# Performance work log

Measured on AMD Instinct MI355X. Metric: run time of the kernel, lower is better.

## Reference

```python
import jax, jax.numpy as jnp
import numpy as np

N_NODES = 50000
N_EDGES = 800000
IN_CH, HID_CH, OUT_CH = 128, 256, 256
N_LAYERS = 3


def setup_inputs() -> dict:
    key = jax.random.key(0)
    ks = jax.random.split(key, 9)
    x = jax.random.normal(ks[0], (N_NODES, IN_CH), dtype=jnp.float32)
    edge_index = jax.random.randint(ks[1], (2, N_EDGES), 0, N_NODES, dtype=jnp.int32)
    # Linear params, Kaiming-ish scale
    W1 = jax.random.normal(ks[2], (IN_CH, HID_CH), dtype=jnp.float32) / np.float32(np.sqrt(IN_CH))
    b1 = jnp.zeros((HID_CH,), jnp.float32)
    W2 = jax.random.normal(ks[3], (HID_CH, HID_CH), dtype=jnp.float32) / np.float32(np.sqrt(HID_CH))
    b2 = jnp.zeros((HID_CH,), jnp.float32)
    W3 = jax.random.normal(ks[4], (HID_CH, OUT_CH), dtype=jnp.float32) / np.float32(np.sqrt(HID_CH))
    b3 = jnp.zeros((OUT_CH,), jnp.float32)
    # learnable eps per GINConv (train_eps=True); small nonzero values for a nontrivial test
    eps = jax.random.normal(ks[5], (N_LAYERS,), dtype=jnp.float32) * 0.01
    return {"x": x, "edge_index": edge_index, "W1": W1, "b1": b1,
            "W2": W2, "b2": b2, "W3": W3, "b3": b3, "eps": eps}


def _gin_conv(x, src, dst, eps, W, b):
    # sum aggregation over incoming edges: agg[i] = sum_{(j->i)} x[j]
    agg = jax.ops.segment_sum(x[src], dst, num_segments=N_NODES)
    h = (1.0 + eps) * x + agg
    return h @ W + b


def reference(x, edge_index, W1, b1, W2, b2, W3, b3, eps):
    src, dst = edge_index[0], edge_index[1]
    # layers 0..L-2: conv -> relu -> dropout (identity in eval mode)
    h = jax.nn.relu(_gin_conv(x, src, dst, eps[0], W1, b1))
    h = jax.nn.relu(_gin_conv(h, src, dst, eps[1], W2, b2))
    # final layer: no relu
    out = _gin_conv(h, src, dst, eps[2], W3, b3)
    return out
```

## Files before the change

kernel.cpp:

```cpp
#include <hip/hip_runtime.h>


typedef __attribute__((ext_vector_type(8))) short short8;
typedef __attribute__((ext_vector_type(4))) float f32x4;

__device__ inline unsigned short f2bf(float f) {
    union { float f; unsigned u; } v; v.f = f;
    unsigned r = v.u + 0x7fffu + ((v.u >> 16) & 1u);
    return (unsigned short)(r >> 16);
}
__device__ inline float bflo(unsigned u) { return __uint_as_float(u << 16); }
__device__ inline float bfhi(unsigned u) { return __uint_as_float(u & 0xffff0000u); }

__device__ __forceinline__ void gload_lds16(const unsigned short* g, unsigned short* l) {
    __builtin_amdgcn_global_load_lds(
        (const __attribute__((address_space(1))) unsigned int*)g,
        (__attribute__((address_space(3))) unsigned int*)l,
        16, 0, 0);
}

#define ACC8(v) { acc[0]+=bflo(v.x); acc[1]+=bfhi(v.x); acc[2]+=bflo(v.y); acc[3]+=bfhi(v.y); \
                  acc[4]+=bflo(v.z); acc[5]+=bfhi(v.z); acc[6]+=bflo(v.w); acc[7]+=bfhi(v.w); }

__global__ __launch_bounds__(256) void prep_kernel(
    const float* __restrict__ x, const int* __restrict__ dst,
    const float* __restrict__ W1, const float* __restrict__ W2,
    const float* __restrict__ W3,
    unsigned short* __restrict__ xb, int* __restrict__ cnt,
    unsigned short* __restrict__ Ws1, unsigned short* __restrict__ Ws2,
    unsigned short* __restrict__ Ws3, int M, int nE)
{
    const int i  = blockIdx.x * 256 + threadIdx.x;
    const int nx = M * 16;
    if (i < nx) {
        const float4* xf = reinterpret_cast<const float4*>(x);
        float4 a = xf[2*i], b = xf[2*i + 1];
        uint4 o;
        o.x = (unsigned)f2bf(a.x) | ((unsigned)f2bf(a.y) << 16);
        o.y = (unsigned)f2bf(a.z) | ((unsigned)f2bf(a.w) << 16);
        o.z = (unsigned)f2bf(b.x) | ((unsigned)f2bf(b.y) << 16);
        o.w = (unsigned)f2bf(b.z) | ((unsigned)f2bf(b.w) << 16);
        reinterpret_cast<uint4*>(xb)[i] = o;
    } else if (i < nx + nE) {
        atomicAdd(&cnt[dst[i - nx]], 1);
    } else {
        int j = i - nx - nE;
        const float* W; unsigned short* D;
        if (j < 32768)       { W = W1; D = Ws1; }
        else if (j < 98304)  { W = W2; D = Ws2; j -= 32768; }
        else if (j < 163840) { W = W3; D = Ws3; j -= 98304; }
        else return;
        const int k = j >> 8, n = j & 255;
        D[((size_t)(k >> 3) * 256 + n) * 8 + (k & 7)] = f2bf(W[(size_t)k * 256 + n]);
    }
}


__global__ __launch_bounds__(1024) void scan1_kernel(
    const int* __restrict__ cnt, int* __restrict__ excl,
    int* __restrict__ bsum, int n)
{
    __shared__ int sh[1024];
    const int tid = threadIdx.x;
    const int i = blockIdx.x * 1024 + tid;
    int v = (i < n) ? cnt[i] : 0;
    sh[tid] = v;
    __syncthreads();
    #pragma unroll
    for (int off = 1; off < 1024; off <<= 1) {
        int t = (tid >= off) ? sh[tid - off] : 0;
        __syncthreads();
        sh[tid] += t;
        __syncthreads();
    }
    if (i < n) excl[i] = sh[tid] - v;
    if (tid == 1023) bsum[blockIdx.x] = sh[1023];
}

__global__ __launch_bounds__(1024) void scan3_kernel(
    const int* __restrict__ excl, const int* __restrict__ bsum,
    int* __restrict__ row_start, int* __restrict__ cursor,
    int n, int nE, int nbl)
{
    __shared__ int sb[64];
    const int tid = threadIdx.x;
    if (tid < 64) sb[tid] = (tid < nbl) ? bsum[tid] : 0;
    __syncthreads();
    #pragma unroll
    for (int off = 1; off < 64; off <<= 1) {
        int v = 0;
        if (tid < 64 && tid >= off) v = sb[tid - off];
        __syncthreads();
        if (tid < 64) sb[tid] += v;
        __syncthreads();
    }
    const int boff = sb[blockIdx.x] - bsum[blockIdx.x];
    const int i = blockIdx.x * 1024 + tid;
    if (i < n) {
        int v = excl[i] + boff;
        row_start[i] = v;
        cursor[i] = v;
    }
    if (i == 0) row_start[n] = nE;
}

__global__ __launch_bounds__(256) void build_adj_kernel(
    const int* __restrict__ src, const int* __restrict__ dst,
    int* __restrict__ cursor, int* __restrict__ adj, int nE)
{
    int e = blockIdx.x * 256 + threadIdx.x;
    if (e < nE) {
        int p = atomicAdd(&cursor[dst[e]], 1);
        adj[p] = src[e];
    }
}


template <int C>
__global__ __launch_bounds__(256) void aggregate_bf16(
    const unsigned short* __restrict__ X, const int* __restrict__ row_start,
    const int* __restrict__ adj, const float* __restrict__ eps_arr, int layer,
    unsigned short* __restrict__ H, int M)
{
    constexpr int TPN = C / 8;
    constexpr int NPB = 256 / TPN;
    const int node = blockIdx.x * NPB + (threadIdx.x / TPN);
    const int c8   = threadIdx.x & (TPN - 1);
    if (node >= M) return;

    const uint4* __restrict__ X4 = reinterpret_cast<const uint4*>(X);

    float acc[8] = {0.f,0.f,0.f,0.f,0.f,0.f,0.f,0.f};
    const int s0 = row_start[node];
    const int s1 = row_start[node + 1];
    const int deg = s1 - s0;

    int j = s0;
    if (deg >= 4) {
        const int jend = s0 + (deg & ~3);
        int a0 = adj[j], a1 = adj[j+1], a2 = adj[j+2], a3 = adj[j+3];
        uint4 p0 = X4[(size_t)a0 * TPN + c8];
        uint4 p1 = X4[(size_t)a1 * TPN + c8];
        uint4 p2 = X4[(size_t)a2 * TPN + c8];
        uint4 p3 = X4[(size_t)a3 * TPN + c8];
        for (j += 4; j < jend; j += 4) {
            const int b0 = adj[j], b1 = adj[j+1], b2 = adj[j+2], b3 = adj[j+3];
            const uint4 n0 = X4[(size_t)b0 * TPN + c8];
            const uint4 n1 = X4[(size_t)b1 * TPN + c8];
            const uint4 n2 = X4[(size_t)b2 * TPN + c8];
            const uint4 n3 = X4[(size_t)b3 * TPN + c8];
            ACC8(p0); ACC8(p1); ACC8(p2); ACC8(p3);
            p0 = n0; p1 = n1; p2 = n2; p3 = n3;
        }
        ACC8(p0); ACC8(p1); ACC8(p2); ACC8(p3);
    }
    for (; j < s1; ++j) {
        uint4 v = X4[(size_t)adj[j] * TPN + c8];
        ACC8(v);
    }

    const uint4 xv = X4[(size_t)node * TPN + c8];
    const float epsv = 1.0f + eps_arr[layer];
    float o[8];
    o[0] = epsv * bflo(xv.x) + acc[0]; o[1] = epsv * bfhi(xv.x) + acc[1];
    o[2] = epsv * bflo(xv.y) + acc[2]; o[3] = epsv * bfhi(xv.y) + acc[3];
    o[4] = epsv * bflo(xv.z) + acc[4]; o[5] = epsv * bfhi(xv.z) + acc[5];
    o[6] = epsv * bflo(xv.w) + acc[6]; o[7] = epsv * bfhi(xv.w) + acc[7];

    uint4 ov;
    ov.x = (unsigned)f2bf(o[0]) | ((unsigned)f2bf(o[1]) << 16);
    ov.y = (unsigned)f2bf(o[2]) | ((unsigned)f2bf(o[3]) << 16);
    ov.z = (unsigned)f2bf(o[4]) | ((unsigned)f2bf(o[5]) << 16);
    ov.w = (unsigned)f2bf(o[6]) | ((unsigned)f2bf(o[7]) << 16);
    reinterpret_cast<uint4*>(H)[(size_t)node * TPN + c8] = ov;
}


template <int CIN, int RELU, int BF16OUT>
__global__ __launch_bounds__(256) void gemm_tiled(
    const unsigned short* __restrict__ H, const unsigned short* __restrict__ Wsub,
    const float* __restrict__ bias, void* __restrict__ out, int M)
{
    constexpr int S = CIN / 32;

    __shared__ __align__(16) unsigned short As[2][4][64][8];

    const int t    = threadIdx.x;
    const int bm   = blockIdx.x * 64;
    const int w    = t >> 6, lane = t & 63;
    const int lr   = lane & 15, ko = lane >> 4;

    const int srow = t & 63;
    const int skb  = t >> 6;
    const unsigned short* aG = H + (size_t)(bm + srow) * CIN + skb * 8;

    f32x4 acc[4][4];
    #pragma unroll
    for (int fn = 0; fn < 4; ++fn) {
        const float bb = bias[w*64 + fn*16 + lr];
        #pragma unroll
        for (int fm = 0; fm < 4; ++fm) {
            acc[fm][fn][0] = bb; acc[fm][fn][1] = bb;
            acc[fm][fn][2] = bb; acc[fm][fn][3] = bb;
        }
    }

    gload_lds16(aG, &As[0][skb][srow][0]);

    int cur = 0;
    for (int s = 0; s < S; ++s) {
        __syncthreads();
        if (s + 1 < S)
            gload_lds16(aG + (s+1)*32, &As[cur ^ 1][skb][srow][0]);

        short8 af[4], bf8[4];
        #pragma unroll
        for (int fm = 0; fm < 4; ++fm)
            af[fm] = *reinterpret_cast<const short8*>(&As[cur][ko][fm*16 + lr][0]);
        #pragma unroll
        for (int fn = 0; fn < 4; ++fn)
            bf8[fn] = *reinterpret_cast<const short8*>(
                Wsub + ((size_t)(s*4 + ko) * 256 + w*64 + fn*16 + lr) * 8);
        #pragma unroll
        for (int fm = 0; fm < 4; ++fm)
            #pragma unroll
            for (int fn = 0; fn < 4; ++fn)
                acc[fm][fn] = __builtin_amdgcn_mfma_f32_16x16x32_bf16(
                    af[fm], bf8[fn], acc[fm][fn], 0, 0, 0);

        cur ^= 1;
    }

    #pragma unroll
    for (int fm = 0; fm < 4; ++fm) {
        #pragma unroll
        for (int fn = 0; fn < 4; ++fn) {
            const int col = w*64 + fn*16 + lr;
            #pragma unroll
            for (int r = 0; r < 4; ++r) {
                const int row = bm + fm*16 + ko*4 + r;
                if (row < M) {
                    float v = acc[fm][fn][r];
                    if (RELU) v = fmaxf(v, 0.f);
                    if (BF16OUT)
                        ((unsigned short*)out)[(size_t)row * 256 + col] = f2bf(v);
                    else
                        ((float*)out)[(size_t)row * 256 + col] = v;
                }
            }
        }
    }
}


extern "C" void kernel_launch(void* const* d_in, const int* in_sizes, int n_in,
                              void* d_out, int out_size, void* d_ws, size_t ws_size,
                              hipStream_t stream)
{
    const float* x   = (const float*)d_in[0];
    const int*   ei  = (const int*)  d_in[1];
    const float* W1  = (const float*)d_in[2];
    const float* b1  = (const float*)d_in[3];
    const float* W2  = (const float*)d_in[4];
    const float* b2  = (const float*)d_in[5];
    const float* W3  = (const float*)d_in[6];
    const float* b3  = (const float*)d_in[7];
    const float* eps = (const float*)d_in[8];

    const int M  = in_sizes[0] / 128;
    const int nE = in_sizes[1] / 2;
    const int Mp = ((M + 63) / 64) * 64;
    const int* srcI = ei;
    const int* dstI = ei + nE;

    char* p = (char*)d_ws;
    unsigned short* xb  = (unsigned short*)p; p += (size_t)Mp * 128 * 2;
    unsigned short* h1  = (unsigned short*)p; p += (size_t)Mp * 256 * 2;
    unsigned short* h2  = (unsigned short*)p; p += (size_t)Mp * 256 * 2;
    unsigned short* Ws1 = (unsigned short*)p; p += (size_t)128 * 256 * 2;
    unsigned short* Ws2 = (unsigned short*)p; p += (size_t)256 * 256 * 2;
    unsigned short* Ws3 = (unsigned short*)p; p += (size_t)256 * 256 * 2;
    int* cnt       = (int*)p; p += (size_t)M * 4;
    int* excl      = (int*)p; p += (size_t)M * 4;
    int* bsum      = (int*)p; p += 64 * 4;
    int* row_start = (int*)p; p += (size_t)(M + 2) * 4;
    int* cursor    = (int*)p; p += (size_t)M * 4;
    int* adj       = (int*)p; p += (size_t)nE * 4;

    const int nbl = (M + 1023) / 1024;

    hipMemsetAsync(cnt, 0, (size_t)M * sizeof(int), stream);
    {
        const int total = M * 16 + nE + 163840;
        prep_kernel<<<(total + 255) / 256, 256, 0, stream>>>(
            x, dstI, W1, W2, W3, xb, cnt, Ws1, Ws2, Ws3, M, nE);
    }
    scan1_kernel<<<nbl, 1024, 0, stream>>>(cnt, excl, bsum, M);
    scan3_kernel<<<nbl, 1024, 0, stream>>>(excl, bsum, row_start, cursor, M, nE, nbl);
    build_adj_kernel<<<(nE + 255) / 256, 256, 0, stream>>>(srcI, dstI, cursor, adj, nE);

    const int gblk = Mp / 64;

    aggregate_bf16<128><<<(M + 15) / 16, 256, 0, stream>>>(
        xb, row_start, adj, eps, 0, h1, M);
    gemm_tiled<128, 1, 1><<<gblk, 256, 0, stream>>>(h1, Ws1, b1, h2, M);

    aggregate_bf16<256><<<(M + 7) / 8, 256, 0, stream>>>(
        h2, row_start, adj, eps, 1, h1, M);
    gemm_tiled<256, 1, 1><<<gblk, 256, 0, stream>>>(h1, Ws2, b2, h2, M);

    aggregate_bf16<256><<<(M + 7) / 8, 256, 0, stream>>>(
        h2, row_start, adj, eps, 2, h1, M);
    gemm_tiled<256, 0, 0><<<gblk, 256, 0, stream>>>(h1, Ws3, b3, d_out, M);
}
```

Baseline: 303.4 us.

## Store node features in channel-sliced layout and aggregate slices per block

Node features are now stored as eight channel slices (each slice holds all nodes contiguously), both in the prep conversion and in the GEMM epilogue. A new aggregation kernel assigns each block one slice and gives each wave a set of nodes, spreading a node's edges across lane groups and combining them with cross-lane shuffle reductions. The intent is that each block gathers from a smaller working set that fits better in L2 or the caches, and that a node's edges are processed in parallel. In exchange each gather becomes an 8-byte load instead of 16 bytes, shuffle reductions are added, and the GEMM's bf16 output is written with a scattered, strided pattern.

```diff
diff --git a/kernel.cpp b/kernel.cpp
--- a/kernel.cpp
+++ b/kernel.cpp
@@ -18,9 +18,6 @@
         (__attribute__((address_space(3))) unsigned int*)l,
         16, 0, 0);
 }
-
-#define ACC8(v) { acc[0]+=bflo(v.x); acc[1]+=bfhi(v.x); acc[2]+=bflo(v.y); acc[3]+=bfhi(v.y); \
-                  acc[4]+=bflo(v.z); acc[5]+=bfhi(v.z); acc[6]+=bflo(v.w); acc[7]+=bfhi(v.w); }
 
 __global__ __launch_bounds__(256) void prep_kernel(
     const float* __restrict__ x, const int* __restrict__ dst,
@@ -40,7 +37,11 @@
         o.y = (unsigned)f2bf(a.z) | ((unsigned)f2bf(a.w) << 16);
         o.z = (unsigned)f2bf(b.x) | ((unsigned)f2bf(b.y) << 16);
         o.w = (unsigned)f2bf(b.z) | ((unsigned)f2bf(b.w) << 16);
-        reinterpret_cast<uint4*>(xb)[i] = o;
+        const int node = i >> 4;
+        const int c0   = (i & 15) * 8;
+        const int cs   = c0 >> 4;
+        const size_t idx = (size_t)cs * M * 16 + (size_t)node * 16 + (c0 & 15);
+        *reinterpret_cast<uint4*>(xb + idx) = o;
     } else if (i < nx + nE) {
         atomicAdd(&cnt[dst[i - nx]], 1);
     } else {
@@ -116,67 +117,66 @@
 }
 
 
-template <int C>
-__global__ __launch_bounds__(256) void aggregate_bf16(
-    const unsigned short* __restrict__ X, const int* __restrict__ row_start,
-    const int* __restrict__ adj, const float* __restrict__ eps_arr, int layer,
+template <int CIN>
+__global__ __launch_bounds__(256) void agg_sliced(
+    const unsigned short* __restrict__ Xcs,
+    const int* __restrict__ row_start, const int* __restrict__ adj,
+    const float* __restrict__ eps_arr, int layer,
     unsigned short* __restrict__ H, int M)
 {
-    constexpr int TPN = C / 8;
-    constexpr int NPB = 256 / TPN;
-    const int node = blockIdx.x * NPB + (threadIdx.x / TPN);
-    const int c8   = threadIdx.x & (TPN - 1);
-    if (node >= M) return;
-
-    const uint4* __restrict__ X4 = reinterpret_cast<const uint4*>(X);
-
-    float acc[8] = {0.f,0.f,0.f,0.f,0.f,0.f,0.f,0.f};
-    const int s0 = row_start[node];
-    const int s1 = row_start[node + 1];
-    const int deg = s1 - s0;
-
-    int j = s0;
-    if (deg >= 4) {
-        const int jend = s0 + (deg & ~3);
-        int a0 = adj[j], a1 = adj[j+1], a2 = adj[j+2], a3 = adj[j+3];
-        uint4 p0 = X4[(size_t)a0 * TPN + c8];
-        uint4 p1 = X4[(size_t)a1 * TPN + c8];
-        uint4 p2 = X4[(size_t)a2 * TPN + c8];
-        uint4 p3 = X4[(size_t)a3 * TPN + c8];
-        for (j += 4; j < jend; j += 4) {
-            const int b0 = adj[j], b1 = adj[j+1], b2 = adj[j+2], b3 = adj[j+3];
-            const uint4 n0 = X4[(size_t)b0 * TPN + c8];
-            const uint4 n1 = X4[(size_t)b1 * TPN + c8];
-            const uint4 n2 = X4[(size_t)b2 * TPN + c8];
-            const uint4 n3 = X4[(size_t)b3 * TPN + c8];
-            ACC8(p0); ACC8(p1); ACC8(p2); ACC8(p3);
-            p0 = n0; p1 = n1; p2 = n2; p3 = n3;
-        }
-        ACC8(p0); ACC8(p1); ACC8(p2); ACC8(p3);
-    }
-    for (; j < s1; ++j) {
-        uint4 v = X4[(size_t)adj[j] * TPN + c8];
-        ACC8(v);
-    }
-
-    const uint4 xv = X4[(size_t)node * TPN + c8];
+    constexpr int SC = CIN / 8;
+    constexpr int CL = SC / 4;
+    constexpr int EG = 64 / CL;
+    constexpr int NW = 8;
+
+    const int cs   = blockIdx.x & 7;
+    const int grp  = blockIdx.x >> 3;
+    const int wave = threadIdx.x >> 6;
+    const int lane = threadIdx.x & 63;
+    const int cl   = lane & (CL - 1);
+    const int eg   = lane / CL;
+
+    const uint2* __restrict__ X2 = reinterpret_cast<const uint2*>(Xcs);
+    const size_t sbase = (size_t)cs * M * CL;
     const float epsv = 1.0f + eps_arr[layer];
-    float o[8];
-    o[0] = epsv * bflo(xv.x) + acc[0]; o[1] = epsv * bfhi(xv.x) + acc[1];
-    o[2] = epsv * bflo(xv.y) + acc[2]; o[3] = epsv * bfhi(xv.y) + acc[3];
-    o[4] = epsv * bflo(xv.z) + acc[4]; o[5] = epsv * bfhi(xv.z) + acc[5];
-    o[6] = epsv * bflo(xv.w) + acc[6]; o[7] = epsv * bfhi(xv.w) + acc[7];
-
-    uint4 ov;
-    ov.x = (unsigned)f2bf(o[0]) | ((unsigned)f2bf(o[1]) << 16);
-    ov.y = (unsigned)f2bf(o[2]) | ((unsigned)f2bf(o[3]) << 16);
-    ov.z = (unsigned)f2bf(o[4]) | ((unsigned)f2bf(o[5]) << 16);
-    ov.w = (unsigned)f2bf(o[6]) | ((unsigned)f2bf(o[7]) << 16);
-    reinterpret_cast<uint4*>(H)[(size_t)node * TPN + c8] = ov;
-}
-
-
-template <int CIN, int RELU, int BF16OUT>
+
+    const int nbase = (grp * 4 + wave) * NW;
+    #pragma unroll 1
+    for (int i = 0; i < NW; ++i) {
+        const int node = nbase + i;
+        if (node >= M) break;
+        const int s0 = row_start[node], s1 = row_start[node + 1];
+
+        float a0 = 0.f, a1 = 0.f, a2 = 0.f, a3 = 0.f;
+        for (int e = s0 + eg; e < s1; e += EG) {
+            const int src = adj[e];
+            const uint2 v = X2[sbase + (size_t)src * CL + cl];
+            a0 += bflo(v.x); a1 += bfhi(v.x);
+            a2 += bflo(v.y); a3 += bfhi(v.y);
+        }
+        #pragma unroll
+        for (int m = CL; m < 64; m <<= 1) {
+            a0 += __shfl_xor(a0, m);
+            a1 += __shfl_xor(a1, m);
+            a2 += __shfl_xor(a2, m);
+            a3 += __shfl_xor(a3, m);
+        }
+        const uint2 xv = X2[sbase + (size_t)node * CL + cl];
+        const float o0 = epsv * bflo(xv.x) + a0;
+        const float o1 = epsv * bfhi(xv.x) + a1;
+        const float o2 = epsv * bflo(xv.y) + a2;
+        const float o3 = epsv * bfhi(xv.y) + a3;
+        if (eg == 0) {
+            uint2 ov;
+            ov.x = (unsigned)f2bf(o0) | ((unsigned)f2bf(o1) << 16);
+            ov.y = (unsigned)f2bf(o2) | ((unsigned)f2bf(o3) << 16);
+            *reinterpret_cast<uint2*>(H + (size_t)node * CIN + cs * SC + cl * 4) = ov;
+        }
+    }
+}
+
+
+template <int CIN, int RELU, int OUTMODE>
 __global__ __launch_bounds__(256) void gemm_tiled(
     const unsigned short* __restrict__ H, const unsigned short* __restrict__ Wsub,
     const float* __restrict__ bias, void* __restrict__ out, int M)
@@ -242,10 +242,12 @@
                 if (row < M) {
                     float v = acc[fm][fn][r];
                     if (RELU) v = fmaxf(v, 0.f);
-                    if (BF16OUT)
-                        ((unsigned short*)out)[(size_t)row * 256 + col] = f2bf(v);
-                    else
+                    if (OUTMODE == 1) {
+                        ((unsigned short*)out)[(size_t)(col >> 5) * M * 32
+                                               + (size_t)row * 32 + (col & 31)] = f2bf(v);
+                    } else {
                         ((float*)out)[(size_t)row * 256 + col] = v;
+                    }
                 }
             }
         }
@@ -274,12 +276,12 @@
     const int* dstI = ei + nE;
 
     char* p = (char*)d_ws;
-    unsigned short* xb  = (unsigned short*)p; p += (size_t)Mp * 128 * 2;
-    unsigned short* h1  = (unsigned short*)p; p += (size_t)Mp * 256 * 2;
-    unsigned short* h2  = (unsigned short*)p; p += (size_t)Mp * 256 * 2;
-    unsigned short* Ws1 = (unsigned short*)p; p += (size_t)128 * 256 * 2;
-    unsigned short* Ws2 = (unsigned short*)p; p += (size_t)256 * 256 * 2;
-    unsigned short* Ws3 = (unsigned short*)p; p += (size_t)256 * 256 * 2;
+    unsigned short* xb_cs = (unsigned short*)p; p += (size_t)M  * 128 * 2;
+    unsigned short* Arow  = (unsigned short*)p; p += (size_t)Mp * 256 * 2;
+    unsigned short* s_cs  = (unsigned short*)p; p += (size_t)M  * 256 * 2;
+    unsigned short* Ws1   = (unsigned short*)p; p += (size_t)128 * 256 * 2;
+    unsigned short* Ws2   = (unsigned short*)p; p += (size_t)256 * 256 * 2;
+    unsigned short* Ws3   = (unsigned short*)p; p += (size_t)256 * 256 * 2;
     int* cnt       = (int*)p; p += (size_t)M * 4;
     int* excl      = (int*)p; p += (size_t)M * 4;
     int* bsum      = (int*)p; p += 64 * 4;
@@ -293,23 +295,21 @@
     {
         const int total = M * 16 + nE + 163840;
         prep_kernel<<<(total + 255) / 256, 256, 0, stream>>>(
-            x, dstI, W1, W2, W3, xb, cnt, Ws1, Ws2, Ws3, M, nE);
+            x, dstI, W1, W2, W3, xb_cs, cnt, Ws1, Ws2, Ws3, M, nE);
     }
     scan1_kernel<<<nbl, 1024, 0, stream>>>(cnt, excl, bsum, M);
     scan3_kernel<<<nbl, 1024, 0, stream>>>(excl, bsum, row_start, cursor, M, nE, nbl);
     build_adj_kernel<<<(nE + 255) / 256, 256, 0, stream>>>(srcI, dstI, cursor, adj, nE);
 
+    const int ablk = 8 * ((M + 31) / 32);
     const int gblk = Mp / 64;
 
-    aggregate_bf16<128><<<(M + 15) / 16, 256, 0, stream>>>(
-        xb, row_start, adj, eps, 0, h1, M);
-    gemm_tiled<128, 1, 1><<<gblk, 256, 0, stream>>>(h1, Ws1, b1, h2, M);
-
-    aggregate_bf16<256><<<(M + 7) / 8, 256, 0, stream>>>(
-        h2, row_start, adj, eps, 1, h1, M);
-    gemm_tiled<256, 1, 1><<<gblk, 256, 0, stream>>>(h1, Ws2, b2, h2, M);
-
-    aggregate_bf16<256><<<(M + 7) / 8, 256, 0, stream>>>(
-        h2, row_start, adj, eps, 2, h1, M);
-    gemm_tiled<256, 0, 0><<<gblk, 256, 0, stream>>>(h1, Ws3, b3, d_out, M);
-}
+    agg_sliced<128><<<ablk, 256, 0, stream>>>(xb_cs, row_start, adj, eps, 0, Arow, M);
+    gemm_tiled<128, 1, 1><<<gblk, 256, 0, stream>>>(Arow, Ws1, b1, s_cs, M);
+
+    agg_sliced<256><<<ablk, 256, 0, stream>>>(s_cs, row_start, adj, eps, 1, Arow, M);
+    gemm_tiled<256, 1, 1><<<gblk, 256, 0, stream>>>(Arow, Ws2, b2, s_cs, M);
+
+    agg_sliced<256><<<ablk, 256, 0, stream>>>(s_cs, row_start, adj, eps, 2, Arow, M);
+    gemm_tiled<256, 0, 0><<<gblk, 256, 0, stream>>>(Arow, Ws3, b3, d_out, M);
+}
```

Measured after the change: 495.2 us. 1.63x slower.
